# Performance work log

Measured on AMD Instinct MI355X. Metric: run time of the kernel, lower is better.

## Reference

```python
import jax, jax.numpy as jnp
import numpy as np

N_NODES, N_EDGES, N_EVAL = 100000, 1600000, 200000
IN_C, HID_C, OUT_C = 128, 256, 128


def setup_inputs() -> dict:
    key = jax.random.key(0)
    ks = jax.random.split(key, 10)
    x = jax.random.normal(ks[0], (N_NODES, IN_C), dtype=jnp.float32)
    edge_index = jax.random.randint(ks[1], (2, N_EDGES), 0, N_NODES)
    pos_edge_index = jax.random.randint(ks[2], (2, N_EVAL), 0, N_NODES)
    neg_edge_index = jax.random.randint(ks[3], (2, N_EVAL), 0, N_NODES)

    def glorot(k, fi, fo):
        return jax.random.normal(k, (fi, fo), dtype=jnp.float32) * np.float32(1.0 / np.sqrt(fi))

    W1 = glorot(ks[4], IN_C, HID_C); b1 = jnp.zeros((HID_C,), jnp.float32)
    W2 = glorot(ks[5], HID_C, HID_C); b2 = jnp.zeros((HID_C,), jnp.float32)
    W3 = glorot(ks[6], HID_C, OUT_C); b3 = jnp.zeros((OUT_C,), jnp.float32)
    return dict(x=x, edge_index=edge_index, pos_edge_index=pos_edge_index,
                neg_edge_index=neg_edge_index, W1=W1, b1=b1, W2=W2, b2=b2, W3=W3, b3=b3)


def gcn_layer(x, W, b, src, dst, deg_inv_sqrt):
    # GCNConv: D^{-1/2} (A + I) D^{-1/2} X W + b, degrees include self-loops.
    h = x @ W                                            # [N, F_out]
    norm = deg_inv_sqrt[src] * deg_inv_sqrt[dst]         # [E]
    msg = h[src] * norm[:, None]                          # [E, F_out] gathered messages
    agg = jax.ops.segment_sum(msg, dst, num_segments=x.shape[0])
    agg = agg + h * (deg_inv_sqrt * deg_inv_sqrt)[:, None]  # self-loop contribution
    return agg + b


def reference(x, edge_index, pos_edge_index, neg_edge_index, W1, b1, W2, b2, W3, b3):
    n = x.shape[0]
    src, dst = edge_index[0], edge_index[1]
    # in-degree with self-loops
    deg = jax.ops.segment_sum(jnp.ones_like(dst, dtype=x.dtype), dst, num_segments=n) + 1.0
    dis = jax.lax.rsqrt(deg)
    # encode (index=0); dropout is identity in eval mode
    h = jax.nn.relu(gcn_layer(x, W1, b1, src, dst, dis))
    h = jax.nn.relu(gcn_layer(h, W2, b2, src, dst, dis))
    z = gcn_layer(h, W3, b3, src, dst, dis)
    # decode: per-edge dot product over pos + neg eval edges
    ei = jnp.concatenate([pos_edge_index, neg_edge_index], axis=1)
    logits = jnp.sum(z[ei[0]] * z[ei[1]], axis=-1)
    return logits
```

## Files before the change

### kernel.cpp

```cpp
#include <hip/hip_runtime.h>
#include <cstdint>
#include <cstddef>

#define N_NODES 100000
#define N_EDGES 1600000
#define N_EVAL  200000

typedef __attribute__((ext_vector_type(8))) short bf16x8;
typedef __attribute__((ext_vector_type(4))) float f32x4;
typedef __attribute__((ext_vector_type(8))) unsigned short u16x8;

__device__ __forceinline__ unsigned short f2bf_rne(float f) {
    unsigned int u = __float_as_uint(f);
    unsigned int r = (u + 0x7FFFu + ((u >> 16) & 1u)) >> 16;
    return (unsigned short)r;
}
__device__ __forceinline__ float bf2f(unsigned short h) {
    return __uint_as_float(((unsigned int)h) << 16);
}


__global__ void count_deg_kernel(const int* __restrict__ dst, int* __restrict__ deg, int E) {
    int i = blockIdx.x * blockDim.x + threadIdx.x;
    if (i < E) atomicAdd(&deg[dst[i]], 1);
}

__global__ void dis_kernel(const int* __restrict__ deg, float* __restrict__ dis, int N) {
    int i = blockIdx.x * blockDim.x + threadIdx.x;
    if (i < N) dis[i] = rsqrtf((float)deg[i] + 1.0f);
}

__global__ __launch_bounds__(1024) void scan_kernel(const int* __restrict__ deg,
                                                    int* __restrict__ offsets, int N, int E) {
    __shared__ int sums[1024];
    int t = threadIdx.x;
    int C = (N + 1023) >> 10;
    int lo = t * C;
    int hi = min(lo + C, N);
    int s = 0;
    for (int i = lo; i < hi; ++i) s += deg[i];
    sums[t] = s;
    __syncthreads();
    for (int d = 1; d < 1024; d <<= 1) {
        int add = (t >= d) ? sums[t - d] : 0;
        __syncthreads();
        sums[t] += add;
        __syncthreads();
    }
    int run = sums[t] - s;
    for (int i = lo; i < hi; ++i) { offsets[i] = run; run += deg[i]; }
    if (hi >= N) offsets[N] = E;
}

__global__ void fill_csr_kernel(const int* __restrict__ src, const int* __restrict__ dst,
                                const float* __restrict__ dis, int* __restrict__ cursor,
                                int2* __restrict__ csr, int E) {
    int e = blockIdx.x * blockDim.x + threadIdx.x;
    if (e < E) {
        int s = src[e], d = dst[e];
        int p = atomicAdd(&cursor[d], 1);
        csr[p] = make_int2(s, __float_as_int(dis[s] * dis[d]));
    }
}


__global__ void wsplit_kernel(const float* __restrict__ W, unsigned short* __restrict__ Wt_hi,
                              unsigned short* __restrict__ Wt_lo, int K, int N) {
    int idx = blockIdx.x * blockDim.x + threadIdx.x;
    if (idx >= K * N) return;
    int k = idx / N, n = idx - k * N;
    float v = W[idx];
    unsigned short h = f2bf_rne(v);
    Wt_hi[(size_t)n * K + k] = h;
    Wt_lo[(size_t)n * K + k] = f2bf_rne(v - bf2f(h));
}


#define KP 40

template <bool BIAS, bool RELU>
__global__ __launch_bounds__(256, 2) void gemm_bf16split_kernel(
    const float* __restrict__ A,
    const unsigned short* __restrict__ Wt_hi,
    const unsigned short* __restrict__ Wt_lo,
    float* __restrict__ C, int M, int N, int K,
    const float* __restrict__ bias)
{
    __shared__ unsigned short As_hi[128][KP];
    __shared__ unsigned short As_lo[128][KP];
    __shared__ unsigned short Bs_hi[128][KP];
    __shared__ unsigned short Bs_lo[128][KP];

    const int tid = threadIdx.x;
    const int m0 = blockIdx.x * 128;
    const int n0 = blockIdx.y * 128;
    const int lane = tid & 63;
    const int wave = tid >> 6;
    const int wm0 = (wave >> 1) * 64;
    const int wn0 = (wave & 1) * 64;
    const int fr = lane & 15;
    const int fk = (lane >> 4) * 8;

    f32x4 acc[4][4];
#pragma unroll
    for (int i = 0; i < 4; ++i)
#pragma unroll
        for (int j = 0; j < 4; ++j) acc[i][j] = (f32x4){0.f, 0.f, 0.f, 0.f};

    const int srow = tid >> 1;
    const int sc0 = (tid & 1) * 16;
    const int agrow = m0 + srow;
    const float* Ap = A + (size_t)agrow * K + sc0;
    const unsigned short* Bh = Wt_hi + (size_t)(n0 + srow) * K + sc0;
    const unsigned short* Bl = Wt_lo + (size_t)(n0 + srow) * K + sc0;

    for (int k0 = 0; k0 < K; k0 += 32) {
        float a[16];
        if (agrow < M) {
            *(float4*)(a)      = *(const float4*)(Ap + k0);
            *(float4*)(a + 4)  = *(const float4*)(Ap + k0 + 4);
            *(float4*)(a + 8)  = *(const float4*)(Ap + k0 + 8);
            *(float4*)(a + 12) = *(const float4*)(Ap + k0 + 12);
        } else {
#pragma unroll
            for (int i = 0; i < 16; ++i) a[i] = 0.f;
        }
        unsigned short h[16], l[16];
#pragma unroll
        for (int i = 0; i < 16; ++i) {
            unsigned short hh = f2bf_rne(a[i]);
            h[i] = hh;
            l[i] = f2bf_rne(a[i] - bf2f(hh));
        }
        *(u16x8*)&As_hi[srow][sc0]     = *(const u16x8*)(h);
        *(u16x8*)&As_hi[srow][sc0 + 8] = *(const u16x8*)(h + 8);
        *(u16x8*)&As_lo[srow][sc0]     = *(const u16x8*)(l);
        *(u16x8*)&As_lo[srow][sc0 + 8] = *(const u16x8*)(l + 8);
        *(u16x8*)&Bs_hi[srow][sc0]     = *(const u16x8*)(Bh + k0);
        *(u16x8*)&Bs_hi[srow][sc0 + 8] = *(const u16x8*)(Bh + k0 + 8);
        *(u16x8*)&Bs_lo[srow][sc0]     = *(const u16x8*)(Bl + k0);
        *(u16x8*)&Bs_lo[srow][sc0 + 8] = *(const u16x8*)(Bl + k0 + 8);
        __syncthreads();

        bf16x8 af_h[4], af_l[4], bf_h[4], bf_l[4];
#pragma unroll
        for (int i = 0; i < 4; ++i) {
            af_h[i] = *(const bf16x8*)&As_hi[wm0 + i * 16 + fr][fk];
            af_l[i] = *(const bf16x8*)&As_lo[wm0 + i * 16 + fr][fk];
            bf_h[i] = *(const bf16x8*)&Bs_hi[wn0 + i * 16 + fr][fk];
            bf_l[i] = *(const bf16x8*)&Bs_lo[wn0 + i * 16 + fr][fk];
        }
#pragma unroll
        for (int i = 0; i < 4; ++i)
#pragma unroll
            for (int j = 0; j < 4; ++j) {
                acc[i][j] = __builtin_amdgcn_mfma_f32_16x16x32_bf16(af_h[i], bf_h[j], acc[i][j], 0, 0, 0);
                acc[i][j] = __builtin_amdgcn_mfma_f32_16x16x32_bf16(af_l[i], bf_h[j], acc[i][j], 0, 0, 0);
                acc[i][j] = __builtin_amdgcn_mfma_f32_16x16x32_bf16(af_h[i], bf_l[j], acc[i][j], 0, 0, 0);
            }
        __syncthreads();
    }

#pragma unroll
    for (int j = 0; j < 4; ++j) {
        const int col = n0 + wn0 + j * 16 + fr;
        const float bb = BIAS ? bias[col] : 0.f;
#pragma unroll
        for (int i = 0; i < 4; ++i) {
            const int rbase = m0 + wm0 + i * 16 + (lane >> 4) * 4;
#pragma unroll
            for (int r = 0; r < 4; ++r) {
                const int row = rbase + r;
                if (row < M) {
                    float v = acc[i][j][r] + bb;
                    if (RELU) v = fmaxf(v, 0.f);
                    C[(size_t)row * N + col] = v;
                }
            }
        }
    }
}


template <int VEC>
__device__ __forceinline__ void vload(float (&r)[VEC], const float* __restrict__ p) {
    if constexpr (VEC == 4) {
        float4 v = *(const float4*)p;
        r[0] = v.x; r[1] = v.y; r[2] = v.z; r[3] = v.w;
    } else {
        float2 v = *(const float2*)p;
        r[0] = v.x; r[1] = v.y;
    }
}

template <int F, bool BIAS, bool RELU>
__global__ __launch_bounds__(256) void aggregate_vec_kernel(
    const float* __restrict__ H,
    const int* __restrict__ offsets,
    const int2* __restrict__ csr,
    const float* __restrict__ dis,
    const float* __restrict__ bias,
    float* __restrict__ OUT, int N)
{
    constexpr int VEC = F / 64;
    const int node = blockIdx.x * 4 + (threadIdx.x >> 6);
    if (node >= N) return;
    const int lane = threadIdx.x & 63;
    const int col = lane * VEC;

    const float d = dis[node];
    float acc[VEC];
    {
        float v[VEC];
        vload<VEC>(v, H + (size_t)node * F + col);
        const float dd = d * d;
#pragma unroll
        for (int q = 0; q < VEC; ++q) acc[q] = v[q] * dd;
    }

    const int e0 = offsets[node], e1 = offsets[node + 1];
    int e = e0;
    for (; e + 8 <= e1; e += 8) {
        int2 c[8];
#pragma unroll
        for (int q = 0; q < 8; ++q) c[q] = csr[e + q];
        float v[8][VEC];
#pragma unroll
        for (int q = 0; q < 8; ++q) vload<VEC>(v[q], H + (size_t)c[q].x * F + col);
#pragma unroll
        for (int q = 0; q < 8; ++q) {
            const float w = __int_as_float(c[q].y);
#pragma unroll
            for (int vv = 0; vv < VEC; ++vv) acc[vv] = fmaf(w, v[q][vv], acc[vv]);
        }
    }
    for (; e + 2 <= e1; e += 2) {
        int2 c0 = csr[e], c1 = csr[e + 1];
        float v0[VEC], v1[VEC];
        vload<VEC>(v0, H + (size_t)c0.x * F + col);
        vload<VEC>(v1, H + (size_t)c1.x * F + col);
        const float w0 = __int_as_float(c0.y), w1 = __int_as_float(c1.y);
#pragma unroll
        for (int q = 0; q < VEC; ++q) acc[q] = fmaf(w0, v0[q], acc[q]);
#pragma unroll
        for (int q = 0; q < VEC; ++q) acc[q] = fmaf(w1, v1[q], acc[q]);
    }
    if (e < e1) {
        int2 c0 = csr[e];
        float v0[VEC];
        vload<VEC>(v0, H + (size_t)c0.x * F + col);
        const float w0 = __int_as_float(c0.y);
#pragma unroll
        for (int q = 0; q < VEC; ++q) acc[q] = fmaf(w0, v0[q], acc[q]);
    }

    if (BIAS) {
        float b[VEC];
        vload<VEC>(b, bias + col);
#pragma unroll
        for (int q = 0; q < VEC; ++q) acc[q] += b[q];
    }
    if (RELU) {
#pragma unroll
        for (int q = 0; q < VEC; ++q) acc[q] = fmaxf(acc[q], 0.f);
    }

    float* op = OUT + (size_t)node * F + col;
    if constexpr (VEC == 4) {
        *(float4*)op = make_float4(acc[0], acc[1], acc[2], acc[3]);
    } else {
        *(float2*)op = make_float2(acc[0], acc[1]);
    }
}


__global__ __launch_bounds__(256) void decode_kernel(const float* __restrict__ z,
                                                     const int* __restrict__ pos,
                                                     const int* __restrict__ neg,
                                                     float* __restrict__ out)
{
    const int wave = threadIdx.x >> 6;
    const int lane = threadIdx.x & 63;
    const int ebase = (blockIdx.x * 4 + wave) * 4;
    if (ebase >= 2 * N_EVAL) return;
    int ia[4], ib[4];
#pragma unroll
    for (int q = 0; q < 4; ++q) {
        const int e = ebase + q;
        if (e < N_EVAL) { ia[q] = pos[e];          ib[q] = pos[N_EVAL + e]; }
        else            { ia[q] = neg[e - N_EVAL]; ib[q] = neg[e]; }
    }
    float2 za[4], zb[4];
#pragma unroll
    for (int q = 0; q < 4; ++q) {
        za[q] = *(const float2*)(z + (size_t)ia[q] * 128 + lane * 2);
        zb[q] = *(const float2*)(z + (size_t)ib[q] * 128 + lane * 2);
    }
    float v[4];
#pragma unroll
    for (int q = 0; q < 4; ++q) v[q] = za[q].x * zb[q].x + za[q].y * zb[q].y;
#pragma unroll
    for (int d = 32; d > 0; d >>= 1) {
#pragma unroll
        for (int q = 0; q < 4; ++q) v[q] += __shfl_xor(v[q], d);
    }
    if (lane == 0) {
#pragma unroll
        for (int q = 0; q < 4; ++q) out[ebase + q] = v[q];
    }
}


extern "C" void kernel_launch(void* const* d_in, const int* in_sizes, int n_in,
                              void* d_out, int out_size, void* d_ws, size_t ws_size,
                              hipStream_t stream)
{
    const float* x  = (const float*)d_in[0];
    const int*   ei = (const int*)d_in[1];
    const int*  pos = (const int*)d_in[2];
    const int*  neg = (const int*)d_in[3];
    const float* W1 = (const float*)d_in[4];
    const float* b1 = (const float*)d_in[5];
    const float* W2 = (const float*)d_in[6];
    const float* b2 = (const float*)d_in[7];
    const float* W3 = (const float*)d_in[8];
    const float* b3 = (const float*)d_in[9];
    float* out = (float*)d_out;

    const int N = N_NODES, E = N_EDGES;

    char* p = (char*)d_ws;
    auto alloc = [&](size_t bytes) {
        char* r = p;
        p += (bytes + 255) & ~(size_t)255;
        return r;
    };
    int*   deg     = (int*)  alloc((size_t)N * 4);
    int*   offsets = (int*)  alloc((size_t)(N + 1) * 4);
    int*   cursor  = (int*)  alloc((size_t)N * 4);
    float* dis     = (float*)alloc((size_t)N * 4);
    int2*  csr     = (int2*) alloc((size_t)E * 8);
    float* P       = (float*)alloc((size_t)N * 256 * 4);
    float* Q       = (float*)alloc((size_t)N * 256 * 4);
    unsigned short* W1h = (unsigned short*)alloc((size_t)256 * 128 * 2);
    unsigned short* W1l = (unsigned short*)alloc((size_t)256 * 128 * 2);
    unsigned short* W2h = (unsigned short*)alloc((size_t)256 * 256 * 2);
    unsigned short* W2l = (unsigned short*)alloc((size_t)256 * 256 * 2);
    unsigned short* W3h = (unsigned short*)alloc((size_t)128 * 256 * 2);
    unsigned short* W3l = (unsigned short*)alloc((size_t)128 * 256 * 2);

    const int* src = ei;
    const int* dst = ei + E;

    wsplit_kernel<<<(128 * 256 + 255) / 256, 256, 0, stream>>>(W1, W1h, W1l, 128, 256);
    wsplit_kernel<<<(256 * 256 + 255) / 256, 256, 0, stream>>>(W2, W2h, W2l, 256, 256);
    wsplit_kernel<<<(256 * 128 + 255) / 256, 256, 0, stream>>>(W3, W3h, W3l, 256, 128);

    hipMemsetAsync(deg, 0, (size_t)N * 4, stream);
    count_deg_kernel<<<(E + 255) / 256, 256, 0, stream>>>(dst, deg, E);
    dis_kernel<<<(N + 255) / 256, 256, 0, stream>>>(deg, dis, N);
    scan_kernel<<<1, 1024, 0, stream>>>(deg, offsets, N, E);
    hipMemcpyAsync(cursor, offsets, (size_t)N * 4, hipMemcpyDeviceToDevice, stream);
    fill_csr_kernel<<<(E + 255) / 256, 256, 0, stream>>>(src, dst, dis, cursor, csr, E);

    const int agg_grid = (N + 3) / 4;
    const int mblocks = (N + 127) / 128;

    aggregate_vec_kernel<128, false, false><<<agg_grid, 256, 0, stream>>>(
        x, offsets, csr, dis, nullptr, P, N);
    gemm_bf16split_kernel<true, true><<<dim3(mblocks, 2), 256, 0, stream>>>(
        P, W1h, W1l, Q, N, 256, 128, b1);

    gemm_bf16split_kernel<false, false><<<dim3(mblocks, 2), 256, 0, stream>>>(
        Q, W2h, W2l, P, N, 256, 256, nullptr);
    aggregate_vec_kernel<256, true, true><<<agg_grid, 256, 0, stream>>>(
        P, offsets, csr, dis, b2, Q, N);

    gemm_bf16split_kernel<false, false><<<dim3(mblocks, 1), 256, 0, stream>>>(
        Q, W3h, W3l, P, N, 128, 256, nullptr);
    float* Z = Q;
    aggregate_vec_kernel<128, true, false><<<agg_grid, 256, 0, stream>>>(
        P, offsets, csr, dis, b3, Z, N);

    decode_kernel<<<(2 * N_EVAL + 15) / 16, 256, 0, stream>>>(Z, pos, neg, out);
}
```

Baseline: 1.005 ms.

## Pre-split GEMM inputs into packed bf16 hi/lo in producer epilogues

Producers of GEMM inputs (aggregation and GEMM epilogues) now write each value as a packed 32-bit hi/lo bf16 pair, so the GEMM A-tile loader only unpacks bits instead of doing the float-to-bf16 split per tile. All intermediate stores become nontemporal. The aggregation inner loop is reduced from 8-wide to 4-wide unrolling with a scalar tail. This moves split arithmetic out of the GEMM main loop, at the cost of fewer outstanding gathers per wave and possible cache effects from the nontemporal stores.

New measurement: 1.040 ms. +3.5%, slower.

```diff
diff --git a/kernel.cpp b/kernel.cpp
--- a/kernel.cpp
+++ b/kernel.cpp
@@ -8,6 +8,9 @@
 
 typedef __attribute__((ext_vector_type(8))) short bf16x8;
 typedef __attribute__((ext_vector_type(4))) float f32x4;
+typedef __attribute__((ext_vector_type(2))) float f32x2;
+typedef __attribute__((ext_vector_type(4))) unsigned int u32x4;
+typedef __attribute__((ext_vector_type(2))) unsigned int u32x2;
 typedef __attribute__((ext_vector_type(8))) unsigned short u16x8;
 
 __device__ __forceinline__ unsigned short f2bf_rne(float f) {
@@ -17,6 +20,11 @@
 }
 __device__ __forceinline__ float bf2f(unsigned short h) {
     return __uint_as_float(((unsigned int)h) << 16);
+}
+__device__ __forceinline__ unsigned int pack_bf(float v) {
+    unsigned short h = f2bf_rne(v);
+    unsigned short l = f2bf_rne(v - bf2f(h));
+    return ((unsigned int)h << 16) | (unsigned int)l;
 }
 
 
@@ -78,12 +86,12 @@
 
 #define KP 40
 
-template <bool BIAS, bool RELU>
+template <bool BIAS, bool RELU, bool PACKOUT>
 __global__ __launch_bounds__(256, 2) void gemm_bf16split_kernel(
-    const float* __restrict__ A,
+    const unsigned int* __restrict__ A,
     const unsigned short* __restrict__ Wt_hi,
     const unsigned short* __restrict__ Wt_lo,
-    float* __restrict__ C, int M, int N, int K,
+    void* __restrict__ Cout, int M, int N, int K,
     const float* __restrict__ bias)
 {
     __shared__ unsigned short As_hi[128][KP];
@@ -110,27 +118,26 @@
     const int srow = tid >> 1;
     const int sc0 = (tid & 1) * 16;
     const int agrow = m0 + srow;
-    const float* Ap = A + (size_t)agrow * K + sc0;
+    const unsigned int* Ap = A + (size_t)agrow * K + sc0;
     const unsigned short* Bh = Wt_hi + (size_t)(n0 + srow) * K + sc0;
     const unsigned short* Bl = Wt_lo + (size_t)(n0 + srow) * K + sc0;
 
     for (int k0 = 0; k0 < K; k0 += 32) {
-        float a[16];
+        unsigned int ua[16];
         if (agrow < M) {
-            *(float4*)(a)      = *(const float4*)(Ap + k0);
-            *(float4*)(a + 4)  = *(const float4*)(Ap + k0 + 4);
-            *(float4*)(a + 8)  = *(const float4*)(Ap + k0 + 8);
-            *(float4*)(a + 12) = *(const float4*)(Ap + k0 + 12);
+            *(u32x4*)(ua)      = *(const u32x4*)(Ap + k0);
+            *(u32x4*)(ua + 4)  = *(const u32x4*)(Ap + k0 + 4);
+            *(u32x4*)(ua + 8)  = *(const u32x4*)(Ap + k0 + 8);
+            *(u32x4*)(ua + 12) = *(const u32x4*)(Ap + k0 + 12);
         } else {
 #pragma unroll
-            for (int i = 0; i < 16; ++i) a[i] = 0.f;
+            for (int i = 0; i < 16; ++i) ua[i] = 0u;
         }
         unsigned short h[16], l[16];
 #pragma unroll
         for (int i = 0; i < 16; ++i) {
-            unsigned short hh = f2bf_rne(a[i]);
-            h[i] = hh;
-            l[i] = f2bf_rne(a[i] - bf2f(hh));
+            h[i] = (unsigned short)(ua[i] >> 16);
+            l[i] = (unsigned short)(ua[i] & 0xFFFFu);
         }
         *(u16x8*)&As_hi[srow][sc0]     = *(const u16x8*)(h);
         *(u16x8*)&As_hi[srow][sc0 + 8] = *(const u16x8*)(h + 8);
@@ -161,6 +168,8 @@
         __syncthreads();
     }
 
+    float* Cf = (float*)Cout;
+    unsigned int* Cp = (unsigned int*)Cout;
 #pragma unroll
     for (int j = 0; j < 4; ++j) {
         const int col = n0 + wn0 + j * 16 + fr;
@@ -174,7 +183,11 @@
                 if (row < M) {
                     float v = acc[i][j][r] + bb;
                     if (RELU) v = fmaxf(v, 0.f);
-                    C[(size_t)row * N + col] = v;
+                    if (PACKOUT) {
+                        __builtin_nontemporal_store(pack_bf(v), &Cp[(size_t)row * N + col]);
+                    } else {
+                        __builtin_nontemporal_store(v, &Cf[(size_t)row * N + col]);
+                    }
                 }
             }
         }
@@ -193,14 +206,14 @@
     }
 }
 
-template <int F, bool BIAS, bool RELU>
+template <int F, bool BIAS, bool RELU, bool PACKOUT>
 __global__ __launch_bounds__(256) void aggregate_vec_kernel(
     const float* __restrict__ H,
     const int* __restrict__ offsets,
     const int2* __restrict__ csr,
     const float* __restrict__ dis,
     const float* __restrict__ bias,
-    float* __restrict__ OUT, int N)
+    void* __restrict__ OUT, int N)
 {
     constexpr int VEC = F / 64;
     const int node = blockIdx.x * 4 + (threadIdx.x >> 6);
@@ -220,32 +233,25 @@
 
     const int e0 = offsets[node], e1 = offsets[node + 1];
     int e = e0;
-    for (; e + 8 <= e1; e += 8) {
-        int2 c[8];
-#pragma unroll
-        for (int q = 0; q < 8; ++q) c[q] = csr[e + q];
-        float v[8][VEC];
-#pragma unroll
-        for (int q = 0; q < 8; ++q) vload<VEC>(v[q], H + (size_t)c[q].x * F + col);
-#pragma unroll
-        for (int q = 0; q < 8; ++q) {
-            const float w = __int_as_float(c[q].y);
-#pragma unroll
-            for (int vv = 0; vv < VEC; ++vv) acc[vv] = fmaf(w, v[q][vv], acc[vv]);
-        }
-    }
-    for (; e + 2 <= e1; e += 2) {
-        int2 c0 = csr[e], c1 = csr[e + 1];
-        float v0[VEC], v1[VEC];
+    for (; e + 4 <= e1; e += 4) {
+        int2 c0 = csr[e], c1 = csr[e + 1], c2 = csr[e + 2], c3 = csr[e + 3];
+        float v0[VEC], v1[VEC], v2[VEC], v3[VEC];
         vload<VEC>(v0, H + (size_t)c0.x * F + col);
         vload<VEC>(v1, H + (size_t)c1.x * F + col);
+        vload<VEC>(v2, H + (size_t)c2.x * F + col);
+        vload<VEC>(v3, H + (size_t)c3.x * F + col);
         const float w0 = __int_as_float(c0.y), w1 = __int_as_float(c1.y);
+        const float w2 = __int_as_float(c2.y), w3 = __int_as_float(c3.y);
 #pragma unroll
         for (int q = 0; q < VEC; ++q) acc[q] = fmaf(w0, v0[q], acc[q]);
 #pragma unroll
         for (int q = 0; q < VEC; ++q) acc[q] = fmaf(w1, v1[q], acc[q]);
-    }
-    if (e < e1) {
+#pragma unroll
+        for (int q = 0; q < VEC; ++q) acc[q] = fmaf(w2, v2[q], acc[q]);
+#pragma unroll
+        for (int q = 0; q < VEC; ++q) acc[q] = fmaf(w3, v3[q], acc[q]);
+    }
+    for (; e < e1; ++e) {
         int2 c0 = csr[e];
         float v0[VEC];
         vload<VEC>(v0, H + (size_t)c0.x * F + col);
@@ -265,11 +271,24 @@
         for (int q = 0; q < VEC; ++q) acc[q] = fmaxf(acc[q], 0.f);
     }
 
-    float* op = OUT + (size_t)node * F + col;
-    if constexpr (VEC == 4) {
-        *(float4*)op = make_float4(acc[0], acc[1], acc[2], acc[3]);
+    if constexpr (PACKOUT) {
+        unsigned int* op = (unsigned int*)OUT + (size_t)node * F + col;
+        if constexpr (VEC == 4) {
+            u32x4 u = {pack_bf(acc[0]), pack_bf(acc[1]), pack_bf(acc[2]), pack_bf(acc[3])};
+            __builtin_nontemporal_store(u, (u32x4*)op);
+        } else {
+            u32x2 u = {pack_bf(acc[0]), pack_bf(acc[1])};
+            __builtin_nontemporal_store(u, (u32x2*)op);
+        }
     } else {
-        *(float2*)op = make_float2(acc[0], acc[1]);
+        float* op = (float*)OUT + (size_t)node * F + col;
+        if constexpr (VEC == 4) {
+            f32x4 v = {acc[0], acc[1], acc[2], acc[3]};
+            __builtin_nontemporal_store(v, (f32x4*)op);
+        } else {
+            f32x2 v = {acc[0], acc[1]};
+            __builtin_nontemporal_store(v, (f32x2*)op);
+        }
     }
 }
 
@@ -340,8 +359,8 @@
     int*   cursor  = (int*)  alloc((size_t)N * 4);
     float* dis     = (float*)alloc((size_t)N * 4);
     int2*  csr     = (int2*) alloc((size_t)E * 8);
-    float* P       = (float*)alloc((size_t)N * 256 * 4);
-    float* Q       = (float*)alloc((size_t)N * 256 * 4);
+    char*  bufA    = (char*) alloc((size_t)N * 256 * 4);
+    char*  bufB    = (char*) alloc((size_t)N * 256 * 4);
     unsigned short* W1h = (unsigned short*)alloc((size_t)256 * 128 * 2);
     unsigned short* W1l = (unsigned short*)alloc((size_t)256 * 128 * 2);
     unsigned short* W2h = (unsigned short*)alloc((size_t)256 * 256 * 2);
@@ -366,21 +385,21 @@
     const int agg_grid = (N + 3) / 4;
     const int mblocks = (N + 127) / 128;
 
-    aggregate_vec_kernel<128, false, false><<<agg_grid, 256, 0, stream>>>(
-        x, offsets, csr, dis, nullptr, P, N);
-    gemm_bf16split_kernel<true, true><<<dim3(mblocks, 2), 256, 0, stream>>>(
-        P, W1h, W1l, Q, N, 256, 128, b1);
-
-    gemm_bf16split_kernel<false, false><<<dim3(mblocks, 2), 256, 0, stream>>>(
-        Q, W2h, W2l, P, N, 256, 256, nullptr);
-    aggregate_vec_kernel<256, true, true><<<agg_grid, 256, 0, stream>>>(
-        P, offsets, csr, dis, b2, Q, N);
-
-    gemm_bf16split_kernel<false, false><<<dim3(mblocks, 1), 256, 0, stream>>>(
-        Q, W3h, W3l, P, N, 128, 256, nullptr);
-    float* Z = Q;
-    aggregate_vec_kernel<128, true, false><<<agg_grid, 256, 0, stream>>>(
-        P, offsets, csr, dis, b3, Z, N);
-
-    decode_kernel<<<(2 * N_EVAL + 15) / 16, 256, 0, stream>>>(Z, pos, neg, out);
-}
+    aggregate_vec_kernel<128, false, false, true><<<agg_grid, 256, 0, stream>>>(
+        x, offsets, csr, dis, nullptr, bufA, N);
+    gemm_bf16split_kernel<true, true, true><<<dim3(mblocks, 2), 256, 0, stream>>>(
+        (const unsigned int*)bufA, W1h, W1l, bufB, N, 256, 128, b1);
+
+    gemm_bf16split_kernel<false, false, false><<<dim3(mblocks, 2), 256, 0, stream>>>(
+        (const unsigned int*)bufB, W2h, W2l, bufA, N, 256, 256, nullptr);
+    aggregate_vec_kernel<256, true, true, true><<<agg_grid, 256, 0, stream>>>(
+        (const float*)bufA, offsets, csr, dis, b2, bufB, N);
+
+    gemm_bf16split_kernel<false, false, false><<<dim3(mblocks, 1), 256, 0, stream>>>(
+        (const unsigned int*)bufB, W3h, W3l, bufA, N, 128, 256, nullptr);
+    aggregate_vec_kernel<128, true, false, false><<<agg_grid, 256, 0, stream>>>(
+        (const float*)bufA, offsets, csr, dis, b3, bufB, N);
+
+    decode_kernel<<<(2 * N_EVAL + 15) / 16, 256, 0, stream>>>(
+        (const float*)bufB, pos, neg, out);
+}
```
